# Optimization experiments

Measured on AMD Instinct MI355X. Metric: run time of the kernel, lower is better.

Reference implementation:

```python
import jax, jax.numpy as jnp
import numpy as np

C = 256
POOL = 4

def setup_inputs() -> dict:
    key = jax.random.key(0)
    ks = jax.random.split(key, 8)
    B, H, W = 4, 256, 256
    d = C // 8
    x = jax.random.normal(ks[0], (B, C, H, W), dtype=jnp.float32)
    # 1x1 conv weights stored as [out, in] matrices (kernel_size=1)
    s = 1.0 / np.sqrt(C)
    Wq = jax.random.uniform(ks[1], (d, C), jnp.float32, -s, s)
    bq = jax.random.uniform(ks[2], (d,), jnp.float32, -s, s)
    Wk = jax.random.uniform(ks[3], (d, C), jnp.float32, -s, s)
    bk = jax.random.uniform(ks[4], (d,), jnp.float32, -s, s)
    Wv = jax.random.uniform(ks[5], (C, C), jnp.float32, -s, s)
    bv = jax.random.uniform(ks[6], (C,), jnp.float32, -s, s)
    gamma = jax.random.normal(ks[7], (1,), jnp.float32) * 0.1
    return {"x": x, "Wq": Wq, "bq": bq, "Wk": Wk, "bk": bk,
            "Wv": Wv, "bv": bv, "gamma": gamma}


def reference(x, Wq, bq, Wk, bk, Wv, bv, gamma):
    B, Cc, H, W = x.shape
    Hp, Wp = H // POOL, W // POOL
    # AvgPool2d(kernel=4, stride=4)
    xp = x.reshape(B, Cc, Hp, POOL, Wp, POOL).mean(axis=(3, 5))  # [B,C,Hp,Wp]
    xf = xp.reshape(B, Cc, Hp * Wp)                              # [B,C,N]
    # 1x1 convs == channel matmuls
    q = jnp.einsum('dc,bcn->bdn', Wq, xf) + bq[None, :, None]    # [B,d,N]
    k = jnp.einsum('dc,bcn->bdn', Wk, xf) + bk[None, :, None]    # [B,d,N]
    v = jnp.einsum('ec,bcn->ben', Wv, xf) + bv[None, :, None]    # [B,C,N]
    # energy[b,n,m] = q[:, :, n] . k[:, :, m]
    energy = jnp.einsum('bdn,bdm->bnm', q, k)                    # [B,N,N]
    attn = jax.nn.softmax(energy, axis=-1)
    # out = v @ attn^T  -> out[b,c,n] = sum_m v[b,c,m] * attn[b,n,m]
    out = jnp.einsum('bcm,bnm->bcn', v, attn)                    # [B,C,N]
    out = out.reshape(B, Cc, Hp, Wp)
    # bilinear upsample, half-pixel centers (align_corners=False)
    up = jax.image.resize(out, (B, Cc, H, W), method='bilinear')
    return gamma[0] * up + x
```

## Files before the change

### kernel.cpp

```cpp
#include <hip/hip_runtime.h>

#define B_ 4
#define C_ 256
#define N_ 4096
#define D_ 32

typedef __bf16 bf16;
typedef __bf16 bf16x4 __attribute__((ext_vector_type(4)));
typedef __bf16 bf16x8 __attribute__((ext_vector_type(8)));
typedef float f32x4 __attribute__((ext_vector_type(4)));

__global__ __launch_bounds__(256) void k_prep(
    const float* __restrict__ Wq, const float* __restrict__ bq,
    const float* __restrict__ Wk, const float* __restrict__ bk,
    const float* __restrict__ Wv, const float* __restrict__ bv,
    bf16* __restrict__ wt, float* __restrict__ bias) {
  int r = blockIdx.x, t = threadIdx.x;
  const float* src; float bval;
  if (r < 32)      { src = Wq + (r << 8);        bval = bq[r]; }
  else if (r < 64) { src = Wk + ((r - 32) << 8); bval = bk[r - 32]; }
  else             { src = Wv + ((r - 64) << 8); bval = bv[r - 64]; }
  wt[(r << 8) + t] = (bf16)src[t];
  if (t == 0) bias[r] = bval;
}

__global__ __launch_bounds__(512) void k_fused(const float* __restrict__ x,
    const bf16* __restrict__ wt, const float* __restrict__ bias,
    bf16* __restrict__ qt, bf16* __restrict__ kt, bf16* __restrict__ v) {
  __shared__ bf16 xsb[32][264];
  int tid = threadIdx.x, wave = tid >> 6, l = tid & 63;
  int lg = l >> 4, ll = l & 15;
  int blk = blockIdx.x;
  int b = blk >> 7, rem = blk & 127, hp = rem >> 1, s = rem & 1;
  int n0 = hp * 64 + s * 32;
  int tok = l & 31, chh = l >> 5;

  const float4* x4 = reinterpret_cast<const float4*>(x) +
      ((size_t)((b * 256 + wave * 32) * 256 + hp * 4)) * 64 + s * 32 + tok;
  for (int c0 = 0; c0 < 32; c0 += 8) {
    float sm[4] = {0.f, 0.f, 0.f, 0.f};
    #pragma unroll
    for (int j = 0; j < 4; ++j) {
      const float4* p = x4 + (size_t)(c0 + chh * 4 + j) * 16384;
      #pragma unroll
      for (int dh = 0; dh < 4; ++dh) {
        float4 a = p[dh * 64];
        sm[j] += a.x + a.y + a.z + a.w;
      }
    }
    bf16x4 pk;
    #pragma unroll
    for (int j = 0; j < 4; ++j) pk[j] = (bf16)(sm[j] * 0.0625f);
    *reinterpret_cast<bf16x4*>(&xsb[tok][wave * 32 + c0 + chh * 4]) = pk;
  }
  __syncthreads();

  f32x4 acc[3][2];
  #pragma unroll
  for (int j = 0; j < 3; ++j)
    #pragma unroll
    for (int cb = 0; cb < 2; ++cb) acc[j][cb] = (f32x4){0.f, 0.f, 0.f, 0.f};

  for (int kk = 0; kk < 8; ++kk) {
    bf16x8 bfr[2];
    #pragma unroll
    for (int cb = 0; cb < 2; ++cb)
      bfr[cb] = *reinterpret_cast<const bf16x8*>(&xsb[cb * 16 + ll][kk * 32 + lg * 8]);
    #pragma unroll
    for (int j = 0; j < 3; ++j) {
      int rb = wave + j * 8;
      if (rb < 20) {
        bf16x8 afr = *reinterpret_cast<const bf16x8*>(
            wt + ((size_t)(rb * 16 + ll)) * 256 + kk * 32 + lg * 8);
        #pragma unroll
        for (int cb = 0; cb < 2; ++cb)
          acc[j][cb] = __builtin_amdgcn_mfma_f32_16x16x32_bf16(afr, bfr[cb], acc[j][cb], 0, 0, 0);
      }
    }
  }

  #pragma unroll
  for (int j = 0; j < 3; ++j) {
    int rb = wave + j * 8;
    if (rb < 20) {
      int row0 = rb * 16 + lg * 4;
      float4 b4 = *reinterpret_cast<const float4*>(bias + row0);
      #pragma unroll
      for (int cb = 0; cb < 2; ++cb) {
        int n = n0 + cb * 16 + ll;
        float v0 = acc[j][cb][0] + b4.x, v1 = acc[j][cb][1] + b4.y;
        float v2 = acc[j][cb][2] + b4.z, v3 = acc[j][cb][3] + b4.w;
        if (row0 < 32) {
          bf16x4 pk = {(bf16)v0, (bf16)v1, (bf16)v2, (bf16)v3};
          *reinterpret_cast<bf16x4*>(qt + ((size_t)(b * N_ + n)) * D_ + row0) = pk;
        } else if (row0 < 64) {
          bf16x4 pk = {(bf16)v0, (bf16)v1, (bf16)v2, (bf16)v3};
          *reinterpret_cast<bf16x4*>(kt + ((size_t)(b * N_ + n)) * D_ + row0 - 32) = pk;
        } else {
          int c = row0 - 64;
          v[((size_t)(b * 256 + c + 0)) * N_ + n] = (bf16)v0;
          v[((size_t)(b * 256 + c + 1)) * N_ + n] = (bf16)v1;
          v[((size_t)(b * 256 + c + 2)) * N_ + n] = (bf16)v2;
          v[((size_t)(b * 256 + c + 3)) * N_ + n] = (bf16)v3;
        }
      }
    }
  }
}

__global__ __launch_bounds__(1024) void k_attn(const bf16* __restrict__ qt,
    const bf16* __restrict__ kt, const bf16* __restrict__ v,
    float* __restrict__ outs) {
  __shared__ bf16 p_s[2][64][256];
  __shared__ float l_red[16][64];
  __shared__ float l_s[64];
  int tid = threadIdx.x, wave = tid >> 6, l = tid & 63;
  int lg = l >> 4, ll = l & 15;
  int blk = blockIdx.x;
  int b  = (blk & 7) >> 1;
  int nt = ((blk >> 3) << 1) | (blk & 1);
  int n0 = nt * 64;

  const f32x4 fz = {0.f, 0.f, 0.f, 0.f};

  bf16x8 aq[4];
  #pragma unroll
  for (int tnf = 0; tnf < 4; ++tnf)
    aq[tnf] = *reinterpret_cast<const bf16x8*>(
        qt + ((size_t)(b * N_ + n0 + tnf * 16 + ll)) * D_ + lg * 8);

  f32x4 acc[4];
  float lsum[4];
  #pragma unroll
  for (int a = 0; a < 4; ++a) { acc[a] = fz; lsum[a] = 0.f; }

  const int mw = wave * 16;
  const int colw = mw + ll;
  const bf16* vbase = v + ((size_t)(b << 8)) * N_;

  const int st_blk = 2 * wave + (lg >> 1);
  const int st_el  = (lg & 1) * 4;

  {
    bf16x8 bk8 = *reinterpret_cast<const bf16x8*>(
        kt + ((size_t)(b * N_ + colw)) * D_ + lg * 8);
    #pragma unroll
    for (int tnf = 0; tnf < 4; ++tnf) {
      f32x4 e = __builtin_amdgcn_mfma_f32_16x16x32_bf16(bk8, aq[tnf], fz, 0, 0, 0);
      int row = tnf * 16 + ll;
      bf16x4 pk;
      #pragma unroll
      for (int r = 0; r < 4; ++r) {
        float p = __expf(e[r]);
        lsum[tnf] += p;
        pk[r] = (bf16)p;
      }
      int col = ((st_blk ^ (row & 7)) << 3) + st_el;
      *reinterpret_cast<bf16x4*>(&p_s[0][row][col]) = pk;
    }
  }
  __syncthreads();

  for (int t = 0; t < 15; ++t) {
    int m0 = t * 256;
    int cur = t & 1, nxt = cur ^ 1;
    bf16x8 bk8 = *reinterpret_cast<const bf16x8*>(
        kt + ((size_t)(b * N_ + m0 + 256 + colw)) * D_ + lg * 8);
    #pragma unroll
    for (int kk = 0; kk < 8; ++kk) {
      bf16x8 bv8 = *reinterpret_cast<const bf16x8*>(
          vbase + ((size_t)colw) * N_ + m0 + kk * 32 + lg * 8);
      #pragma unroll
      for (int tnf = 0; tnf < 4; ++tnf) {
        int row = tnf * 16 + ll;
        int col = (((kk * 4 + lg) ^ (ll & 7)) << 3);
        bf16x8 pa = *reinterpret_cast<const bf16x8*>(&p_s[cur][row][col]);
        acc[tnf] = __builtin_amdgcn_mfma_f32_16x16x32_bf16(pa, bv8, acc[tnf], 0, 0, 0);
      }
    }
    #pragma unroll
    for (int tnf = 0; tnf < 4; ++tnf) {
      f32x4 e = __builtin_amdgcn_mfma_f32_16x16x32_bf16(bk8, aq[tnf], fz, 0, 0, 0);
      int row = tnf * 16 + ll;
      bf16x4 pk;
      #pragma unroll
      for (int r = 0; r < 4; ++r) {
        float p = __expf(e[r]);
        lsum[tnf] += p;
        pk[r] = (bf16)p;
      }
      int col = ((st_blk ^ (row & 7)) << 3) + st_el;
      *reinterpret_cast<bf16x4*>(&p_s[nxt][row][col]) = pk;
    }
    __syncthreads();
  }
  {
    int m0 = 15 * 256;
    #pragma unroll
    for (int kk = 0; kk < 8; ++kk) {
      bf16x8 bv8 = *reinterpret_cast<const bf16x8*>(
          vbase + ((size_t)colw) * N_ + m0 + kk * 32 + lg * 8);
      #pragma unroll
      for (int tnf = 0; tnf < 4; ++tnf) {
        int row = tnf * 16 + ll;
        int col = (((kk * 4 + lg) ^ (ll & 7)) << 3);
        bf16x8 pa = *reinterpret_cast<const bf16x8*>(&p_s[1][row][col]);
        acc[tnf] = __builtin_amdgcn_mfma_f32_16x16x32_bf16(pa, bv8, acc[tnf], 0, 0, 0);
      }
    }
  }

  #pragma unroll
  for (int tnf = 0; tnf < 4; ++tnf) {
    float s = lsum[tnf];
    s += __shfl_xor(s, 16);
    s += __shfl_xor(s, 32);
    if (l < 16) l_red[wave][tnf * 16 + l] = s;
  }
  __syncthreads();
  if (tid < 64) {
    float s = 0.f;
    #pragma unroll
    for (int w = 0; w < 16; ++w) s += l_red[w][tid];
    l_s[tid] = s;
  }
  __syncthreads();

  #pragma unroll
  for (int tnf = 0; tnf < 4; ++tnf) {
    int tn0 = tnf * 16 + lg * 4;
    float4 o;
    o.x = acc[tnf][0] / l_s[tn0 + 0];
    o.y = acc[tnf][1] / l_s[tn0 + 1];
    o.z = acc[tnf][2] / l_s[tn0 + 2];
    o.w = acc[tnf][3] / l_s[tn0 + 3];
    *reinterpret_cast<float4*>(outs + ((size_t)((b << 8) + colw)) * N_ + n0 + tn0) = o;
  }
}

__global__ __launch_bounds__(256) void k_up(const float* __restrict__ outs,
    const float* __restrict__ x, const float* __restrict__ gamma,
    float* __restrict__ out) {
  __shared__ float s_o[4096];
  int tid = threadIdx.x, wave = tid >> 6, tw = tid & 63;
  int bc = blockIdx.x;
  const float* src = outs + (size_t)bc * 4096;
  #pragma unroll
  for (int ch = 0; ch < 4; ++ch)
    *reinterpret_cast<float4*>(&s_o[ch * 1024 + tid * 4]) =
        *reinterpret_cast<const float4*>(src + ch * 1024 + tid * 4);
  __syncthreads();

  float g = gamma[0];
  const float4* xr = reinterpret_cast<const float4*>(x) + (size_t)bc * 16384;
  float4* outr = reinterpret_cast<float4*>(out) + (size_t)bc * 16384;

  int twm = tw == 0 ? 0 : tw - 1;
  int twp = tw == 63 ? 63 : tw + 1;

  for (int hb = 0; hb < 64; ++hb) {
    int h = hb * 4 + wave;
    int th = 2 * h - 3;
    int h0 = th < 0 ? -1 : (th >> 3);
    float fh = (float)(th - 8 * h0) * 0.125f;
    int i0h = h0 < 0 ? 0 : h0;
    int i1h = h0 + 1 > 63 ? 63 : h0 + 1;
    const float* r0 = &s_o[i0h * 64];
    const float* r1 = &s_o[i1h * 64];
    float a_m = r0[twm], a_c = r0[tw], a_p = r0[twp];
    float b_m = r1[twm], b_c = r1[tw], b_p = r1[twp];
    float t0 = a_m + 0.625f * (a_c - a_m), u0 = b_m + 0.625f * (b_c - b_m);
    float t1 = a_m + 0.875f * (a_c - a_m), u1 = b_m + 0.875f * (b_c - b_m);
    float t2 = a_c + 0.125f * (a_p - a_c), u2 = b_c + 0.125f * (b_p - b_c);
    float t3 = a_c + 0.375f * (a_p - a_c), u3 = b_c + 0.375f * (b_p - b_c);
    float4 xv = xr[h * 64 + tw];
    float4 o;
    o.x = g * (t0 + fh * (u0 - t0)) + xv.x;
    o.y = g * (t1 + fh * (u1 - t1)) + xv.y;
    o.z = g * (t2 + fh * (u2 - t2)) + xv.z;
    o.w = g * (t3 + fh * (u3 - t3)) + xv.w;
    outr[h * 64 + tw] = o;
  }
}

extern "C" void kernel_launch(void* const* d_in, const int* in_sizes, int n_in,
                              void* d_out, int out_size, void* d_ws, size_t ws_size,
                              hipStream_t stream) {
  const float* x     = (const float*)d_in[0];
  const float* Wq    = (const float*)d_in[1];
  const float* bq    = (const float*)d_in[2];
  const float* Wk    = (const float*)d_in[3];
  const float* bk    = (const float*)d_in[4];
  const float* Wv    = (const float*)d_in[5];
  const float* bv    = (const float*)d_in[6];
  const float* gamma = (const float*)d_in[7];
  float* out = (float*)d_out;

  char* ws = (char*)d_ws;
  float* outs = (float*)(ws);
  bf16*  v    = (bf16*) (ws + (16u << 20));
  bf16*  qt   = (bf16*) (ws + (24u << 20));
  bf16*  kt   = (bf16*) (ws + (25u << 20));
  bf16*  wt   = (bf16*) (ws + (26u << 20));
  float* bias = (float*)(ws + (27u << 20));

  hipLaunchKernelGGL(k_prep,  dim3(320),  dim3(256),  0, stream,
                     Wq, bq, Wk, bk, Wv, bv, wt, bias);
  hipLaunchKernelGGL(k_fused, dim3(512),  dim3(512),  0, stream,
                     x, wt, bias, qt, kt, v);
  hipLaunchKernelGGL(k_attn,  dim3(256),  dim3(1024), 0, stream, qt, kt, v, outs);
  hipLaunchKernelGGL(k_up,    dim3(1024), dim3(256),  0, stream, outs, x, gamma, out);
}
```

Before: 250.2 us.

## Split attention key dimension across two blocks and combine partials in upsample

The attention kernel now splits the 4096 keys into two halves handled by separate blocks, doubling the grid from 256 to 512 blocks. Each block writes unnormalized partial outputs and partial row sums, and the upsample kernel adds the two partials and divides before interpolating. This is meant to fill more of the GPU's compute units, since 256 blocks of 1024 threads underuse the device. The cost is twice the fp32 output traffic plus extra partial-sum reads. The workspace is reshuffled so the weight and bias buffers overlap outs0, which is safe only because k_fused finishes reading them before k_attn writes there.

```diff
diff --git a/kernel.cpp b/kernel.cpp
--- a/kernel.cpp
+++ b/kernel.cpp
@@ -110,16 +110,18 @@
 
 __global__ __launch_bounds__(1024) void k_attn(const bf16* __restrict__ qt,
     const bf16* __restrict__ kt, const bf16* __restrict__ v,
-    float* __restrict__ outs) {
+    float* __restrict__ outs0, float* __restrict__ outs1,
+    float* __restrict__ lp) {
   __shared__ bf16 p_s[2][64][256];
   __shared__ float l_red[16][64];
-  __shared__ float l_s[64];
   int tid = threadIdx.x, wave = tid >> 6, l = tid & 63;
   int lg = l >> 4, ll = l & 15;
   int blk = blockIdx.x;
   int b  = (blk & 7) >> 1;
-  int nt = ((blk >> 3) << 1) | (blk & 1);
+  int mh = blk & 1;
+  int nt = blk >> 3;
   int n0 = nt * 64;
+  float* outp = mh ? outs1 : outs0;
 
   const f32x4 fz = {0.f, 0.f, 0.f, 0.f};
 
@@ -140,10 +142,11 @@
 
   const int st_blk = 2 * wave + (lg >> 1);
   const int st_el  = (lg & 1) * 4;
+  const int t0 = mh * 8;
 
   {
     bf16x8 bk8 = *reinterpret_cast<const bf16x8*>(
-        kt + ((size_t)(b * N_ + colw)) * D_ + lg * 8);
+        kt + ((size_t)(b * N_ + t0 * 256 + colw)) * D_ + lg * 8);
     #pragma unroll
     for (int tnf = 0; tnf < 4; ++tnf) {
       f32x4 e = __builtin_amdgcn_mfma_f32_16x16x32_bf16(bk8, aq[tnf], fz, 0, 0, 0);
@@ -161,9 +164,10 @@
   }
   __syncthreads();
 
-  for (int t = 0; t < 15; ++t) {
+  for (int i = 0; i < 7; ++i) {
+    int t = t0 + i;
     int m0 = t * 256;
-    int cur = t & 1, nxt = cur ^ 1;
+    int cur = i & 1, nxt = cur ^ 1;
     bf16x8 bk8 = *reinterpret_cast<const bf16x8*>(
         kt + ((size_t)(b * N_ + m0 + 256 + colw)) * D_ + lg * 8);
     #pragma unroll
@@ -195,7 +199,7 @@
     __syncthreads();
   }
   {
-    int m0 = 15 * 256;
+    int m0 = (t0 + 7) * 256;
     #pragma unroll
     for (int kk = 0; kk < 8; ++kk) {
       bf16x8 bv8 = *reinterpret_cast<const bf16x8*>(
@@ -222,33 +226,44 @@
     float s = 0.f;
     #pragma unroll
     for (int w = 0; w < 16; ++w) s += l_red[w][tid];
-    l_s[tid] = s;
-  }
-  __syncthreads();
+    lp[((size_t)(mh * 4 + b)) * N_ + n0 + tid] = s;
+  }
 
   #pragma unroll
   for (int tnf = 0; tnf < 4; ++tnf) {
     int tn0 = tnf * 16 + lg * 4;
     float4 o;
-    o.x = acc[tnf][0] / l_s[tn0 + 0];
-    o.y = acc[tnf][1] / l_s[tn0 + 1];
-    o.z = acc[tnf][2] / l_s[tn0 + 2];
-    o.w = acc[tnf][3] / l_s[tn0 + 3];
-    *reinterpret_cast<float4*>(outs + ((size_t)((b << 8) + colw)) * N_ + n0 + tn0) = o;
-  }
-}
-
-__global__ __launch_bounds__(256) void k_up(const float* __restrict__ outs,
+    o.x = acc[tnf][0]; o.y = acc[tnf][1]; o.z = acc[tnf][2]; o.w = acc[tnf][3];
+    *reinterpret_cast<float4*>(outp + ((size_t)((b << 8) + colw)) * N_ + n0 + tn0) = o;
+  }
+}
+
+__global__ __launch_bounds__(256) void k_up(const float* __restrict__ outs0,
+    const float* __restrict__ outs1, const float* __restrict__ lp,
     const float* __restrict__ x, const float* __restrict__ gamma,
     float* __restrict__ out) {
   __shared__ float s_o[4096];
   int tid = threadIdx.x, wave = tid >> 6, tw = tid & 63;
   int bc = blockIdx.x;
-  const float* src = outs + (size_t)bc * 4096;
-  #pragma unroll
-  for (int ch = 0; ch < 4; ++ch)
-    *reinterpret_cast<float4*>(&s_o[ch * 1024 + tid * 4]) =
-        *reinterpret_cast<const float4*>(src + ch * 1024 + tid * 4);
+  int b = bc >> 8;
+  const float* o0 = outs0 + (size_t)bc * 4096;
+  const float* o1 = outs1 + (size_t)bc * 4096;
+  const float* l0 = lp + (size_t)b * N_;
+  const float* l1 = lp + (size_t)(4 + b) * N_;
+  #pragma unroll
+  for (int ch = 0; ch < 4; ++ch) {
+    int idx = ch * 1024 + tid * 4;
+    float4 a0 = *reinterpret_cast<const float4*>(o0 + idx);
+    float4 a1 = *reinterpret_cast<const float4*>(o1 + idx);
+    float4 s0 = *reinterpret_cast<const float4*>(l0 + idx);
+    float4 s1 = *reinterpret_cast<const float4*>(l1 + idx);
+    float4 r;
+    r.x = (a0.x + a1.x) / (s0.x + s1.x);
+    r.y = (a0.y + a1.y) / (s0.y + s1.y);
+    r.z = (a0.z + a1.z) / (s0.z + s1.z);
+    r.w = (a0.w + a1.w) / (s0.w + s1.w);
+    *reinterpret_cast<float4*>(&s_o[idx]) = r;
+  }
   __syncthreads();
 
   float g = gamma[0];
@@ -297,17 +312,21 @@
   float* out = (float*)d_out;
 
   char* ws = (char*)d_ws;
-  float* outs = (float*)(ws);
-  bf16*  v    = (bf16*) (ws + (16u << 20));
-  bf16*  qt   = (bf16*) (ws + (24u << 20));
-  bf16*  kt   = (bf16*) (ws + (25u << 20));
-  bf16*  wt   = (bf16*) (ws + (26u << 20));
-  float* bias = (float*)(ws + (27u << 20));
+  bf16*  wt    = (bf16*) (ws);
+  float* bias  = (float*)(ws + (200u << 10));
+  float* outs0 = (float*)(ws);
+  float* outs1 = (float*)(ws + (16u << 20));
+  bf16*  v     = (bf16*) (ws + (32u << 20));
+  bf16*  qt    = (bf16*) (ws + (40u << 20));
+  bf16*  kt    = (bf16*) (ws + (41u << 20));
+  float* lpart = (float*)(ws + (42u << 20));
 
   hipLaunchKernelGGL(k_prep,  dim3(320),  dim3(256),  0, stream,
                      Wq, bq, Wk, bk, Wv, bv, wt, bias);
   hipLaunchKernelGGL(k_fused, dim3(512),  dim3(512),  0, stream,
                      x, wt, bias, qt, kt, v);
-  hipLaunchKernelGGL(k_attn,  dim3(256),  dim3(1024), 0, stream, qt, kt, v, outs);
-  hipLaunchKernelGGL(k_up,    dim3(1024), dim3(256),  0, stream, outs, x, gamma, out);
-}
+  hipLaunchKernelGGL(k_attn,  dim3(512),  dim3(1024), 0, stream,
+                     qt, kt, v, outs0, outs1, lpart);
+  hipLaunchKernelGGL(k_up,    dim3(1024), dim3(256),  0, stream,
+                     outs0, outs1, lpart, x, gamma, out);
+}
```

Measured after the change: 252.7 us. Within noise of the previous version (+1.0%).
